# Kernel optimization log

Hardware: AMD Instinct MI355X
Metric: run time of the kernel (lower is better)

## Reference

```python
import jax, jax.numpy as jnp
import numpy as np

N = 262144      # total tokens (rows of batch)
D = 256         # d_model
S = 512         # number of distinct sequence ids
MAX_LEN = 640   # static upper bound on tokens per sequence (counts ~ Binomial(N, 1/S))


def setup_inputs() -> dict:
    key = jax.random.key(0)
    k1, k2 = jax.random.split(key)
    batch = jax.random.normal(k1, (N, D), dtype=jnp.float32)
    sequence_ids = jax.random.randint(k2, (N,), 0, S, dtype=jnp.int32)
    return {"batch": batch, "sequence_ids": sequence_ids}


def reference(batch, sequence_ids):
    # Counting-sort style grouping: for each row, compute its rank within its
    # sequence-id group (preserving original order, like torch.nonzero order),
    # then scatter into a padded [S, MAX_LEN, D] tensor.
    ids = sequence_ids
    ones = jnp.ones((N,), jnp.int32)
    counts = jax.ops.segment_sum(ones, ids, num_segments=S)          # [S]
    offsets = jnp.cumsum(counts) - counts                             # start of each group in sorted order
    order = jnp.argsort(ids)                                          # stable sort by id -> original order within group
    ranks_sorted = jnp.arange(N, dtype=jnp.int32) - offsets[ids[order]]
    ranks = jnp.zeros((N,), jnp.int32).at[order].set(ranks_sorted)    # rank of each row within its group
    padded = jnp.zeros((S, MAX_LEN, D), batch.dtype).at[ids, ranks].set(batch)
    padding_mask = jnp.all(padded == 0, axis=-1)                      # [S, MAX_LEN]
    return padded, padding_mask
```

## Files before the change

### kernel.cpp

```cpp
#include <hip/hip_runtime.h>

#define N_TOK   262144
#define D       256
#define NSEQ    512
#define MAX_LEN 640

#define CHUNK   256
#define NBLK    (N_TOK / CHUNK)
#define SEG     16
#define NSEGS   (NBLK / SEG)

__global__ __launch_bounds__(512) void k_count(const int* __restrict__ ids,
                                               int* __restrict__ counts,
                                               int* __restrict__ segsum) {
    __shared__ int h[SEG][NSEQ];
    const int seg = blockIdx.x;
    const int t   = threadIdx.x;
#pragma unroll
    for (int k = 0; k < SEG; ++k) h[k][t] = 0;
    __syncthreads();
    const int base = seg * (SEG * CHUNK);
#pragma unroll
    for (int k = 0; k < 8; ++k) {
        const int i  = t + 512 * k;
        const int id = ids[base + i];
        atomicAdd(&h[i >> 8][id], 1);
    }
    __syncthreads();
    int acc = 0;
#pragma unroll
    for (int k = 0; k < SEG; ++k) {
        const int c = h[k][t];
        counts[(seg * SEG + k) * NSEQ + t] = c;
        acc += c;
    }
    segsum[seg * NSEQ + t] = acc;
}

__global__ __launch_bounds__(512) void k_expand2(const int* __restrict__ counts,
                                                 const int* __restrict__ segsum,
                                                 int* __restrict__ prefix,
                                                 int* __restrict__ totals) {
    const int seg = blockIdx.x;
    const int t   = threadIdx.x;
    int acc = 0;
    for (int g = 0; g < seg; ++g) acc += segsum[g * NSEQ + t];
#pragma unroll
    for (int k = 0; k < SEG; ++k) {
        const int b = seg * SEG + k;
        prefix[b * NSEQ + t] = acc;
        acc += counts[b * NSEQ + t];
    }
    if (seg == NSEGS - 1) totals[t] = acc;
}

__global__ __launch_bounds__(256) void k_scatter_zero(const float* __restrict__ batch,
                                                      const int* __restrict__ ids,
                                                      const int* __restrict__ prefix,
                                                      const int* __restrict__ totals,
                                                      float* __restrict__ padded,
                                                      float* __restrict__ mask) {
    const int t = threadIdx.x;
    if (blockIdx.x < NBLK) {
        __shared__ int lid[CHUNK];
        __shared__ int pre[NSEQ];
        __shared__ int drow[CHUNK];
        const int b = blockIdx.x;

        lid[t]       = ids[b * CHUNK + t];
        pre[t]       = prefix[b * NSEQ + t];
        pre[t + 256] = prefix[b * NSEQ + t + 256];
        __syncthreads();

        const int myid = lid[t];
        int r = 0;
        for (int j = 0; j < t; ++j) r += (lid[j] == myid);
        r += pre[myid];
        drow[t] = (r < MAX_LEN) ? (myid * MAX_LEN + r) : -1;
        __syncthreads();

        const int wave = t >> 6;
        const int lane = t & 63;
#pragma unroll 8
        for (int r2 = 0; r2 < 64; ++r2) {
            const int row = wave * 64 + r2;
            const float4 v =
                ((const float4*)(batch + (size_t)(b * CHUNK + row) * D))[lane];
            const int dr = drow[row];
            if (dr >= 0)
                ((float4*)(padded + (size_t)dr * D))[lane] = v;
        }
    } else {
        const int s   = blockIdx.x - NBLK;
        const int tot = totals[s];
        const int wave = t >> 6;
        const int lane = t & 63;
        const float4 z = make_float4(0.f, 0.f, 0.f, 0.f);
        for (int l = tot + wave; l < MAX_LEN; l += 4) {
            ((float4*)(padded + (size_t)(s * MAX_LEN + l) * D))[lane] = z;
        }
        for (int l = t; l < MAX_LEN; l += 256) {
            mask[s * MAX_LEN + l] = (l >= tot) ? 1.0f : 0.0f;
        }
    }
}

extern "C" void kernel_launch(void* const* d_in, const int* in_sizes, int n_in,
                              void* d_out, int out_size, void* d_ws, size_t ws_size,
                              hipStream_t stream) {
    const float* batch = (const float*)d_in[0];
    const int*   ids   = (const int*)d_in[1];

    float* padded = (float*)d_out;
    float* mask   = padded + (size_t)NSEQ * MAX_LEN * D;

    int* ws     = (int*)d_ws;
    int* counts = ws;
    int* prefix = counts + NBLK * NSEQ;
    int* segsum = prefix + NBLK * NSEQ;
    int* totals = segsum + NSEGS * NSEQ;

    k_count      <<<NSEGS,       512, 0, stream>>>(ids, counts, segsum);
    k_expand2    <<<NSEGS,       512, 0, stream>>>(counts, segsum, prefix, totals);
    k_scatter_zero<<<NBLK + NSEQ, 256, 0, stream>>>(batch, ids, prefix, totals,
                                                    padded, mask);
}
```

Before: 155.3 us.

## Replace row scatter with index scatter plus output-ordered gather kernel

```diff
diff --git a/kernel.cpp b/kernel.cpp
--- a/kernel.cpp
+++ b/kernel.cpp
@@ -9,6 +9,7 @@
 #define NBLK    (N_TOK / CHUNK)
 #define SEG     16
 #define NSEGS   (NBLK / SEG)
+#define NSLOTS  (NSEQ * MAX_LEN)
 
 __global__ __launch_bounds__(512) void k_count(const int* __restrict__ ids,
                                                int* __restrict__ counts,
@@ -54,54 +55,48 @@
     if (seg == NSEGS - 1) totals[t] = acc;
 }
 
-__global__ __launch_bounds__(256) void k_scatter_zero(const float* __restrict__ batch,
-                                                      const int* __restrict__ ids,
-                                                      const int* __restrict__ prefix,
-                                                      const int* __restrict__ totals,
-                                                      float* __restrict__ padded,
-                                                      float* __restrict__ mask) {
+__global__ __launch_bounds__(256) void k_rankscat(const int* __restrict__ ids,
+                                                  const int* __restrict__ prefix,
+                                                  int* __restrict__ row_index) {
+    __shared__ int lid[CHUNK];
+    __shared__ int pre[NSEQ];
+    const int b = blockIdx.x;
     const int t = threadIdx.x;
-    if (blockIdx.x < NBLK) {
-        __shared__ int lid[CHUNK];
-        __shared__ int pre[NSEQ];
-        __shared__ int drow[CHUNK];
-        const int b = blockIdx.x;
 
-        lid[t]       = ids[b * CHUNK + t];
-        pre[t]       = prefix[b * NSEQ + t];
-        pre[t + 256] = prefix[b * NSEQ + t + 256];
-        __syncthreads();
+    lid[t]       = ids[b * CHUNK + t];
+    pre[t]       = prefix[b * NSEQ + t];
+    pre[t + 256] = prefix[b * NSEQ + t + 256];
+    __syncthreads();
 
-        const int myid = lid[t];
-        int r = 0;
-        for (int j = 0; j < t; ++j) r += (lid[j] == myid);
-        r += pre[myid];
-        drow[t] = (r < MAX_LEN) ? (myid * MAX_LEN + r) : -1;
-        __syncthreads();
+    const int myid = lid[t];
+    int r = 0;
+    for (int j = 0; j < t; ++j) r += (lid[j] == myid);
+    r += pre[myid];
+    if (r < MAX_LEN)
+        row_index[myid * MAX_LEN + r] = b * CHUNK + t;
+}
 
-        const int wave = t >> 6;
-        const int lane = t & 63;
-#pragma unroll 8
-        for (int r2 = 0; r2 < 64; ++r2) {
-            const int row = wave * 64 + r2;
-            const float4 v =
-                ((const float4*)(batch + (size_t)(b * CHUNK + row) * D))[lane];
-            const int dr = drow[row];
-            if (dr >= 0)
-                ((float4*)(padded + (size_t)dr * D))[lane] = v;
+__global__ __launch_bounds__(256) void k_gather(const float* __restrict__ batch,
+                                                const int* __restrict__ row_index,
+                                                const int* __restrict__ totals,
+                                                float* __restrict__ padded,
+                                                float* __restrict__ mask) {
+    const int wid  = (blockIdx.x * 256 + threadIdx.x) >> 6;
+    const int lane = threadIdx.x & 63;
+    const int base = wid * 40;
+#pragma unroll 4
+    for (int i = 0; i < 40; ++i) {
+        const int slot = base + i;
+        const int s    = slot / MAX_LEN;
+        const int l    = slot - s * MAX_LEN;
+        const int tot  = totals[s];
+        float4 v = make_float4(0.f, 0.f, 0.f, 0.f);
+        if (l < tot) {
+            const int r = row_index[slot];
+            v = ((const float4*)(batch + (size_t)r * D))[lane];
         }
-    } else {
-        const int s   = blockIdx.x - NBLK;
-        const int tot = totals[s];
-        const int wave = t >> 6;
-        const int lane = t & 63;
-        const float4 z = make_float4(0.f, 0.f, 0.f, 0.f);
-        for (int l = tot + wave; l < MAX_LEN; l += 4) {
-            ((float4*)(padded + (size_t)(s * MAX_LEN + l) * D))[lane] = z;
-        }
-        for (int l = t; l < MAX_LEN; l += 256) {
-            mask[s * MAX_LEN + l] = (l >= tot) ? 1.0f : 0.0f;
-        }
+        ((float4*)(padded + (size_t)slot * D))[lane] = v;
+        if (lane == 0) mask[slot] = (l >= tot) ? 1.0f : 0.0f;
     }
 }
 
@@ -114,14 +109,15 @@
     float* padded = (float*)d_out;
     float* mask   = padded + (size_t)NSEQ * MAX_LEN * D;
 
-    int* ws     = (int*)d_ws;
-    int* counts = ws;
-    int* prefix = counts + NBLK * NSEQ;
-    int* segsum = prefix + NBLK * NSEQ;
-    int* totals = segsum + NSEGS * NSEQ;
+    int* ws        = (int*)d_ws;
+    int* counts    = ws;
+    int* prefix    = counts + NBLK * NSEQ;
+    int* segsum    = prefix + NBLK * NSEQ;
+    int* totals    = segsum + NSEGS * NSEQ;
+    int* row_index = totals + NSEQ;
 
-    k_count      <<<NSEGS,       512, 0, stream>>>(ids, counts, segsum);
-    k_expand2    <<<NSEGS,       512, 0, stream>>>(counts, segsum, prefix, totals);
-    k_scatter_zero<<<NBLK + NSEQ, 256, 0, stream>>>(batch, ids, prefix, totals,
-                                                    padded, mask);
+    k_count   <<<NSEGS, 512, 0, stream>>>(ids, counts, segsum);
+    k_expand2 <<<NSEGS, 512, 0, stream>>>(counts, segsum, prefix, totals);
+    k_rankscat<<<NBLK,  256, 0, stream>>>(ids, prefix, row_index);
+    k_gather  <<<2048,  256, 0, stream>>>(batch, row_index, totals, padded, mask);
 }
```

After: 160.4 us. 3.3% more time.
